# Kernel tuning notes

Hardware: AMD Instinct MI355X
Metric: run time of the kernel (lower is better)

Reference implementation:

```python
import jax, jax.numpy as jnp
import numpy as np

N, E = 50000, 800000
IN_DIM, HID, ZDIM = 256, 128, 64
LN_EPS = 1e-5


def _layernorm(x, gamma, beta):
    mu = jnp.mean(x, axis=-1, keepdims=True)
    var = jnp.mean(jnp.square(x - mu), axis=-1, keepdims=True)
    return (x - mu) * jax.lax.rsqrt(var + LN_EPS) * gamma + beta


def _gcn_conv(h, src, dst, dinv, W, b):
    # h: (N, d_in) -> (N, d_out). GCNConv: X W, then sym-normalized
    # aggregation over edges with self-loops, then bias.
    h = h @ W                                   # (N, d_out)
    coef = dinv[src] * dinv[dst]                # (E,)
    agg = jax.ops.segment_sum(h[src] * coef[:, None], dst,
                              num_segments=h.shape[0])
    agg = agg + h * jnp.square(dinv)[:, None]   # self-loop term
    return agg + b


def setup_inputs() -> dict:
    key = jax.random.key(0)
    ks = jax.random.split(key, 5)
    x = jax.random.normal(ks[0], (N, IN_DIM), dtype=jnp.float32)
    edge_index = jax.random.randint(ks[1], (2, E), 0, N, dtype=jnp.int64)
    s1 = 1.0 / np.sqrt(IN_DIM)
    s2 = 1.0 / np.sqrt(HID)
    return {
        "x": x,
        "edge_index": edge_index,
        "ln_gamma": jnp.ones((IN_DIM,), jnp.float32),
        "ln_beta": jnp.zeros((IN_DIM,), jnp.float32),
        "W1": jax.random.normal(ks[2], (IN_DIM, HID), jnp.float32) * s1,
        "b1": jnp.zeros((HID,), jnp.float32),
        "W2": jax.random.normal(ks[3], (HID, HID), jnp.float32) * s2,
        "b2": jnp.zeros((HID,), jnp.float32),
        "W3": jax.random.normal(ks[4], (HID, ZDIM), jnp.float32) * s2,
        "b3": jnp.zeros((ZDIM,), jnp.float32),
    }


def reference(x, edge_index, ln_gamma, ln_beta, W1, b1, W2, b2, W3, b3):
    src, dst = edge_index[0], edge_index[1]
    n = x.shape[0]
    # degree with self-loops (dropout is inference no-op, training=False)
    deg = jnp.ones((n,), x.dtype).at[dst].add(1.0)
    dinv = jax.lax.rsqrt(deg)
    h = _layernorm(x, ln_gamma, ln_beta)
    h = jax.nn.relu(_gcn_conv(h, src, dst, dinv, W1, b1))
    h = jax.nn.relu(_gcn_conv(h, src, dst, dinv, W2, b2))
    z = _gcn_conv(h, src, dst, dinv, W3, b3)
    return z
```

## Files before the change

kernel.cpp:

```cpp
#include <hip/hip_runtime.h>
#include <cstdint>
#include <cstddef>


typedef __attribute__((ext_vector_type(8))) __bf16 bf16x8;
typedef __attribute__((ext_vector_type(4))) float f32x4;
typedef _Float16 half_t;
typedef __attribute__((ext_vector_type(8))) _Float16 half8_t;

__global__ void zero_ctl(int* __restrict__ p, int n) {
  int i = blockIdx.x * 256 + threadIdx.x;
  if (i < n) p[i] = 0;
}

__global__ __launch_bounds__(256) void hist_bucket(const int* __restrict__ dst,
                                                   int* __restrict__ bcnt, int E, int NB) {
  __shared__ int h[256];
  int t = threadIdx.x;
  h[t] = 0;
  __syncthreads();
  for (int e = blockIdx.x * 256 + t; e < E; e += gridDim.x * 256)
    atomicAdd(&h[dst[e] >> 8], 1);
  __syncthreads();
  if (t < NB && h[t]) atomicAdd(&bcnt[t], h[t]);
}

__global__ __launch_bounds__(256) void scan_buckets(const int* __restrict__ bcnt,
                                                    int* __restrict__ bbase,
                                                    int* __restrict__ bcur, int NB, int E) {
  __shared__ int tmp[256];
  int t = threadIdx.x;
  int v = (t < NB) ? bcnt[t] : 0;
  tmp[t] = v;
  __syncthreads();
  for (int off = 1; off < 256; off <<= 1) {
    int x = (t >= off) ? tmp[t - off] : 0;
    __syncthreads();
    tmp[t] += x;
    __syncthreads();
  }
  int excl = tmp[t] - v;
  if (t < NB) { bbase[t] = excl; bcur[t] = excl; }
  if (t == 0) bbase[NB] = E;
}

#define CHUNK 4096
__global__ __launch_bounds__(256) void scatter_bins(const int* __restrict__ src,
                                                    const int* __restrict__ dst,
                                                    int* __restrict__ bcur,
                                                    int2* __restrict__ binned, int E) {
  __shared__ int2 recs[CHUNK];
  __shared__ int hist[256], lbase[256], resv[256], cur[256];
  int t = threadIdx.x;
  int e0 = blockIdx.x * CHUNK;
  if (e0 >= E) return;
  int len = min(CHUNK, E - e0);
  hist[t] = 0;
  cur[t] = 0;
  __syncthreads();
  for (int i = t; i < len; i += 256) atomicAdd(&hist[dst[e0 + i] >> 8], 1);
  __syncthreads();
  int v = hist[t];
  lbase[t] = v;
  __syncthreads();
  for (int off = 1; off < 256; off <<= 1) {
    int x = (t >= off) ? lbase[t - off] : 0;
    __syncthreads();
    lbase[t] += x;
    __syncthreads();
  }
  int myexcl = lbase[t] - v;
  if (v) resv[t] = atomicAdd(&bcur[t], v);
  __syncthreads();
  lbase[t] = myexcl;
  __syncthreads();
  for (int i = t; i < len; i += 256) {
    int d = dst[e0 + i], s = src[e0 + i];
    int b = d >> 8;
    int r = atomicAdd(&cur[b], 1);
    recs[lbase[b] + r] = make_int2(s, d);
  }
  __syncthreads();
  for (int i = t; i < len; i += 256) {
    int2 rc = recs[i];
    int b = rc.y >> 8;
    binned[resv[b] + (i - lbase[b])] = rc;
  }
}

#define MAXB 8192
__global__ __launch_bounds__(256) void sort_bucket(const int2* __restrict__ binned,
                                                   const int* __restrict__ bbase,
                                                   int* __restrict__ srcs,
                                                   int* __restrict__ offs,
                                                   float* __restrict__ dinv,
                                                   int N, int NB, int E) {
  __shared__ int2 recs[MAXB];
  __shared__ unsigned short rnk[MAXB];
  __shared__ int sstage[MAXB];
  __shared__ int hist[256], nbase[256];
  int b = blockIdx.x, t = threadIdx.x;
  int base = bbase[b], end = bbase[b + 1];
  int L = end - base;
  if (L > MAXB) L = MAXB;
  hist[t] = 0;
  __syncthreads();
  for (int i = t; i < L; i += 256) {
    int2 rc = binned[base + i];
    recs[i] = rc;
    int r = atomicAdd(&hist[rc.y & 255], 1);
    rnk[i] = (unsigned short)r;
  }
  __syncthreads();
  int v = hist[t];
  nbase[t] = v;
  __syncthreads();
  for (int off = 1; off < 256; off <<= 1) {
    int x = (t >= off) ? nbase[t - off] : 0;
    __syncthreads();
    nbase[t] += x;
    __syncthreads();
  }
  int excl = nbase[t] - v;
  __syncthreads();
  nbase[t] = excl;
  int node = (b << 8) + t;
  if (node < N) {
    offs[node] = base + excl;
    dinv[node] = rsqrtf(1.0f + (float)v);
  }
  if (b == NB - 1 && t == 0) offs[N] = E;
  __syncthreads();
  for (int i = t; i < L; i += 256) {
    int2 rc = recs[i];
    sstage[nbase[rc.y & 255] + rnk[i]] = rc.x;
  }
  __syncthreads();
  for (int i = t; i < L; i += 256) srcs[base + i] = sstage[i];
}

__global__ void fill_w(const int* __restrict__ srcs, const float* __restrict__ dinv,
                       int2* __restrict__ edges, int E) {
  int e = blockIdx.x * 256 + threadIdx.x;
  if (e < E) {
    int s = srcs[e];
    edges[e] = make_int2(s, __float_as_int(dinv[s]));
  }
}

__global__ void ln_stats(const float* __restrict__ x, float* __restrict__ mu,
                         float* __restrict__ rs, int n) {
  int gid = blockIdx.x * blockDim.x + threadIdx.x;
  int wv = gid >> 6, lane = gid & 63;
  if (wv >= n) return;
  const float4* row = (const float4*)(x + (size_t)wv * 256);
  float4 v = row[lane];
  float s = v.x + v.y + v.z + v.w;
  float s2 = v.x * v.x + v.y * v.y + v.z * v.z + v.w * v.w;
  for (int off = 32; off > 0; off >>= 1) {
    s += __shfl_down(s, off);
    s2 += __shfl_down(s2, off);
  }
  if (lane == 0) {
    float m = s * (1.0f / 256.0f);
    float var = s2 * (1.0f / 256.0f) - m * m;
    mu[wv] = m;
    rs[wv] = rsqrtf(var + 1e-5f);
  }
}

__global__ void wsplit(const float* __restrict__ W, unsigned short* __restrict__ Wt_hi,
                       unsigned short* __restrict__ Wt_lo, int K, int NOUT) {
  int idx = blockIdx.x * 256 + threadIdx.x;
  if (idx >= K * NOUT) return;
  int k = idx / NOUT, n = idx % NOUT;
  float v = W[idx];
  __bf16 h = (__bf16)v;
  __bf16 l = (__bf16)(v - (float)h);
  Wt_hi[(size_t)n * K + k] = __builtin_bit_cast(unsigned short, h);
  Wt_lo[(size_t)n * K + k] = __builtin_bit_cast(unsigned short, l);
}

template <int K, int NOUT, bool LN, bool A_FP16>
__launch_bounds__(256)
__global__ void gemm_mfma(const void* __restrict__ Avoid,
                          const unsigned short* __restrict__ Wt_hi,
                          const unsigned short* __restrict__ Wt_lo,
                          const float* __restrict__ mu, const float* __restrict__ rs,
                          const float* __restrict__ gamma, const float* __restrict__ beta,
                          half_t* __restrict__ out, int nrows) {
  constexpr int BM = 64, BK = 32;
  constexpr int NT = NOUT / 16;
  __shared__ unsigned short As_hi[BM][BK];
  __shared__ unsigned short As_lo[BM][BK];
  __shared__ unsigned short Bs_hi[NOUT][BK];
  __shared__ unsigned short Bs_lo[NOUT][BK];

  const int tid = threadIdx.x;
  const int lane = tid & 63;
  const int w = tid >> 6;
  const int quad = lane >> 4;
  const int l16 = lane & 15;
  const int row0 = blockIdx.x * BM;

  f32x4 acc[NT];
#pragma unroll
  for (int t = 0; t < NT; ++t) acc[t] = (f32x4){0.f, 0.f, 0.f, 0.f};

  for (int k0 = 0; k0 < K; k0 += BK) {
    if (!A_FP16) {
      const float* A = (const float*)Avoid;
#pragma unroll
      for (int i = 0; i < 2; ++i) {
        int r = i * 32 + (tid >> 3);
        int c4 = (tid & 7) * 4;
        int grow = row0 + r;
        if (grow > nrows - 1) grow = nrows - 1;
        float4 v = *(const float4*)&A[(size_t)grow * K + k0 + c4];
        if (LN) {
          float m = mu[grow], s = rs[grow];
          float4 g = *(const float4*)&gamma[k0 + c4];
          float4 b = *(const float4*)&beta[k0 + c4];
          v.x = (v.x - m) * s * g.x + b.x;
          v.y = (v.y - m) * s * g.y + b.y;
          v.z = (v.z - m) * s * g.z + b.z;
          v.w = (v.w - m) * s * g.w + b.w;
        }
        float vv[4] = {v.x, v.y, v.z, v.w};
#pragma unroll
        for (int j = 0; j < 4; ++j) {
          __bf16 h = (__bf16)vv[j];
          __bf16 l = (__bf16)(vv[j] - (float)h);
          As_hi[r][c4 + j] = __builtin_bit_cast(unsigned short, h);
          As_lo[r][c4 + j] = __builtin_bit_cast(unsigned short, l);
        }
      }
    } else {
      const half_t* A = (const half_t*)Avoid;
      int r = tid >> 2;
      int c8 = (tid & 3) * 8;
      int grow = row0 + r;
      if (grow > nrows - 1) grow = nrows - 1;
      half8_t v = *(const half8_t*)&A[(size_t)grow * K + k0 + c8];
#pragma unroll
      for (int j = 0; j < 8; ++j) {
        float f = (float)v[j];
        __bf16 h = (__bf16)f;
        __bf16 l = (__bf16)(f - (float)h);
        As_hi[r][c8 + j] = __builtin_bit_cast(unsigned short, h);
        As_lo[r][c8 + j] = __builtin_bit_cast(unsigned short, l);
      }
    }
#pragma unroll
    for (int i = 0; i < NOUT / 64; ++i) {
      int n = i * 64 + (tid >> 2);
      int c8 = (tid & 3) * 8;
      *(uint4*)&Bs_hi[n][c8] = *(const uint4*)&Wt_hi[(size_t)n * K + k0 + c8];
      *(uint4*)&Bs_lo[n][c8] = *(const uint4*)&Wt_lo[(size_t)n * K + k0 + c8];
    }
    __syncthreads();

    bf16x8 ah = *(const bf16x8*)&As_hi[w * 16 + l16][quad * 8];
    bf16x8 al = *(const bf16x8*)&As_lo[w * 16 + l16][quad * 8];
#pragma unroll
    for (int t = 0; t < NT; ++t) {
      bf16x8 bh = *(const bf16x8*)&Bs_hi[t * 16 + l16][quad * 8];
      bf16x8 bl = *(const bf16x8*)&Bs_lo[t * 16 + l16][quad * 8];
      acc[t] = __builtin_amdgcn_mfma_f32_16x16x32_bf16(ah, bh, acc[t], 0, 0, 0);
      acc[t] = __builtin_amdgcn_mfma_f32_16x16x32_bf16(al, bh, acc[t], 0, 0, 0);
      acc[t] = __builtin_amdgcn_mfma_f32_16x16x32_bf16(ah, bl, acc[t], 0, 0, 0);
    }
    __syncthreads();
  }

#pragma unroll
  for (int t = 0; t < NT; ++t) {
#pragma unroll
    for (int r = 0; r < 4; ++r) {
      int grow = row0 + w * 16 + quad * 4 + r;
      if (grow < nrows) out[(size_t)grow * NOUT + t * 16 + l16] = (half_t)acc[t][r];
    }
  }
}

__global__ __launch_bounds__(256) void agg128_h(const half_t* __restrict__ t,
                                                const int* __restrict__ offs,
                                                const int2* __restrict__ edges,
                                                const float* __restrict__ dinv,
                                                const float* __restrict__ bias,
                                                half_t* __restrict__ out, int n) {
  int gid = blockIdx.x * blockDim.x + threadIdx.x;
  int node = gid >> 6, lane = gid & 63;
  if (node >= n) return;
  int qw = lane >> 4;
  int fl = lane & 15;
  int e0 = offs[node], e1 = offs[node + 1];
  float acc[8] = {0.f, 0.f, 0.f, 0.f, 0.f, 0.f, 0.f, 0.f};
  int e = e0 + qw;
  for (; e + 12 < e1; e += 16) {
    int2 da = edges[e], db = edges[e + 4], dc = edges[e + 8], dd = edges[e + 12];
    half8_t va = *(const half8_t*)(t + ((size_t)da.x << 7) + fl * 8);
    half8_t vb = *(const half8_t*)(t + ((size_t)db.x << 7) + fl * 8);
    half8_t vc = *(const half8_t*)(t + ((size_t)dc.x << 7) + fl * 8);
    half8_t vd = *(const half8_t*)(t + ((size_t)dd.x << 7) + fl * 8);
    float wa = __int_as_float(da.y), wb = __int_as_float(db.y);
    float wc = __int_as_float(dc.y), wd = __int_as_float(dd.y);
#pragma unroll
    for (int j = 0; j < 8; ++j) {
      acc[j] = fmaf(wa, (float)va[j], acc[j]);
      acc[j] = fmaf(wb, (float)vb[j], acc[j]);
      acc[j] = fmaf(wc, (float)vc[j], acc[j]);
      acc[j] = fmaf(wd, (float)vd[j], acc[j]);
    }
  }
  for (; e < e1; e += 4) {
    int2 d = edges[e];
    half8_t v = *(const half8_t*)(t + ((size_t)d.x << 7) + fl * 8);
    float w = __int_as_float(d.y);
#pragma unroll
    for (int j = 0; j < 8; ++j) acc[j] = fmaf(w, (float)v[j], acc[j]);
  }
#pragma unroll
  for (int j = 0; j < 8; ++j) {
    acc[j] += __shfl_xor(acc[j], 16);
    acc[j] += __shfl_xor(acc[j], 32);
  }
  if (qw == 0) {
    float di = dinv[node];
    float dii = di * di;
    half8_t sv = *(const half8_t*)(t + ((size_t)node << 7) + fl * 8);
    float4 b0 = *(const float4*)(bias + fl * 8);
    float4 b1 = *(const float4*)(bias + fl * 8 + 4);
    float bb[8] = {b0.x, b0.y, b0.z, b0.w, b1.x, b1.y, b1.z, b1.w};
    half8_t o;
#pragma unroll
    for (int j = 0; j < 8; ++j) {
      float v = di * acc[j] + dii * (float)sv[j] + bb[j];
      o[j] = (half_t)fmaxf(v, 0.f);
    }
    *(half8_t*)(out + ((size_t)node << 7) + fl * 8) = o;
  }
}

__global__ __launch_bounds__(256) void agg64_h(const half_t* __restrict__ t,
                                               const int* __restrict__ offs,
                                               const int2* __restrict__ edges,
                                               const float* __restrict__ dinv,
                                               const float* __restrict__ bias,
                                               float* __restrict__ out, int n) {
  int gid = blockIdx.x * blockDim.x + threadIdx.x;
  int node = gid >> 6, lane = gid & 63;
  if (node >= n) return;
  int og = lane >> 3;
  int fl = lane & 7;
  int e0 = offs[node], e1 = offs[node + 1];
  float acc[8] = {0.f, 0.f, 0.f, 0.f, 0.f, 0.f, 0.f, 0.f};
  int e = e0 + og;
  for (; e + 8 < e1; e += 16) {
    int2 da = edges[e], db = edges[e + 8];
    half8_t va = *(const half8_t*)(t + ((size_t)da.x << 6) + fl * 8);
    half8_t vb = *(const half8_t*)(t + ((size_t)db.x << 6) + fl * 8);
    float wa = __int_as_float(da.y), wb = __int_as_float(db.y);
#pragma unroll
    for (int j = 0; j < 8; ++j) {
      acc[j] = fmaf(wa, (float)va[j], acc[j]);
      acc[j] = fmaf(wb, (float)vb[j], acc[j]);
    }
  }
  for (; e < e1; e += 8) {
    int2 d = edges[e];
    half8_t v = *(const half8_t*)(t + ((size_t)d.x << 6) + fl * 8);
    float w = __int_as_float(d.y);
#pragma unroll
    for (int j = 0; j < 8; ++j) acc[j] = fmaf(w, (float)v[j], acc[j]);
  }
#pragma unroll
  for (int j = 0; j < 8; ++j) {
    acc[j] += __shfl_xor(acc[j], 8);
    acc[j] += __shfl_xor(acc[j], 16);
    acc[j] += __shfl_xor(acc[j], 32);
  }
  if (og == 0) {
    float di = dinv[node];
    float dii = di * di;
    half8_t sv = *(const half8_t*)(t + ((size_t)node << 6) + fl * 8);
    float4 b0 = *(const float4*)(bias + fl * 8);
    float4 b1 = *(const float4*)(bias + fl * 8 + 4);
    float bb[8] = {b0.x, b0.y, b0.z, b0.w, b1.x, b1.y, b1.z, b1.w};
    float4 o0, o1;
    float ov[8];
#pragma unroll
    for (int j = 0; j < 8; ++j) ov[j] = di * acc[j] + dii * (float)sv[j] + bb[j];
    o0 = make_float4(ov[0], ov[1], ov[2], ov[3]);
    o1 = make_float4(ov[4], ov[5], ov[6], ov[7]);
    *(float4*)(out + ((size_t)node << 6) + fl * 8) = o0;
    *(float4*)(out + ((size_t)node << 6) + fl * 8 + 4) = o1;
  }
}

extern "C" void kernel_launch(void* const* d_in, const int* in_sizes, int n_in,
                              void* d_out, int out_size, void* d_ws, size_t ws_size,
                              hipStream_t stream) {
  const float* x = (const float*)d_in[0];
  const int* ei = (const int*)d_in[1];
  const float* gamma = (const float*)d_in[2];
  const float* beta = (const float*)d_in[3];
  const float* W1 = (const float*)d_in[4];
  const float* b1 = (const float*)d_in[5];
  const float* W2 = (const float*)d_in[6];
  const float* b2 = (const float*)d_in[7];
  const float* W3 = (const float*)d_in[8];
  const float* b3 = (const float*)d_in[9];
  float* out = (float*)d_out;

  const int N = in_sizes[0] / 256;
  const int E = in_sizes[1] / 2;
  const int* src = ei;
  const int* dst = ei + E;
  const int NB = (N + 255) >> 8;

  char* ws = (char*)d_ws;
  auto alloc = [&](size_t bytes) -> char* {
    char* p = ws;
    ws += (bytes + 255) & ~(size_t)255;
    return p;
  };
  int* bcnt = (int*)alloc(256 * 4);
  int* bbase = (int*)alloc(257 * 4);
  int* bcur = (int*)alloc(256 * 4);
  int2* binned = (int2*)alloc((size_t)E * 8);
  int* srcs = (int*)alloc((size_t)E * 4);
  int* offs = (int*)alloc((size_t)(N + 1) * 4);
  float* dinv = (float*)alloc((size_t)N * 4);
  int2* edges = (int2*)alloc((size_t)E * 8);
  float* mu = (float*)alloc((size_t)N * 4);
  float* rs = (float*)alloc((size_t)N * 4);
  half_t* t = (half_t*)alloc((size_t)N * 128 * 2);
  half_t* h = (half_t*)alloc((size_t)N * 128 * 2);
  unsigned short* W1t_hi = (unsigned short*)alloc(256 * 128 * 2);
  unsigned short* W1t_lo = (unsigned short*)alloc(256 * 128 * 2);
  unsigned short* W2t_hi = (unsigned short*)alloc(128 * 128 * 2);
  unsigned short* W2t_lo = (unsigned short*)alloc(128 * 128 * 2);
  unsigned short* W3t_hi = (unsigned short*)alloc(128 * 64 * 2);
  unsigned short* W3t_lo = (unsigned short*)alloc(128 * 64 * 2);

  zero_ctl<<<1, 256, 0, stream>>>(bcnt, 256);
  hist_bucket<<<256, 256, 0, stream>>>(dst, bcnt, E, NB);
  scan_buckets<<<1, 256, 0, stream>>>(bcnt, bbase, bcur, NB, E);
  scatter_bins<<<(E + CHUNK - 1) / CHUNK, 256, 0, stream>>>(src, dst, bcur, binned, E);
  sort_bucket<<<NB, 256, 0, stream>>>(binned, bbase, srcs, offs, dinv, N, NB, E);
  fill_w<<<(E + 255) / 256, 256, 0, stream>>>(srcs, dinv, edges, E);

  wsplit<<<(256 * 128 + 255) / 256, 256, 0, stream>>>(W1, W1t_hi, W1t_lo, 256, 128);
  wsplit<<<(128 * 128 + 255) / 256, 256, 0, stream>>>(W2, W2t_hi, W2t_lo, 128, 128);
  wsplit<<<(128 * 64 + 255) / 256, 256, 0, stream>>>(W3, W3t_hi, W3t_lo, 128, 64);

  ln_stats<<<(N + 3) / 4, 256, 0, stream>>>(x, mu, rs, N);

  const int gemm_blocks = (N + 63) / 64;
  const int agg_blocks = (N + 3) / 4;

  gemm_mfma<256, 128, true, false><<<gemm_blocks, 256, 0, stream>>>(
      x, W1t_hi, W1t_lo, mu, rs, gamma, beta, t, N);
  agg128_h<<<agg_blocks, 256, 0, stream>>>(t, offs, edges, dinv, b1, h, N);

  gemm_mfma<128, 128, false, true><<<gemm_blocks, 256, 0, stream>>>(
      h, W2t_hi, W2t_lo, nullptr, nullptr, nullptr, nullptr, t, N);
  agg128_h<<<agg_blocks, 256, 0, stream>>>(t, offs, edges, dinv, b2, h, N);

  gemm_mfma<128, 64, false, true><<<gemm_blocks, 256, 0, stream>>>(
      h, W3t_hi, W3t_lo, nullptr, nullptr, nullptr, nullptr, t, N);
  agg64_h<<<agg_blocks, 256, 0, stream>>>(t, offs, edges, dinv, b3, out, N);
}
```

Before: 301.8 us.

## Fuse LN stats into GEMM, fold edge weights into sort, merge weight splits

Layer-norm row statistics are now computed inside the first GEMM block from the tile's own rows, which removes the separate ln_stats pass and the mu/rs arrays. Degrees are counted with global atomics during the histogram pass so dinv is ready before sorting. That lets sort_bucket write (src, dinv[src]) edge records directly and drops the fill_w kernel and the srcs buffer. The three weight-split launches are merged into one. In exchange, the GEMM re-reads each row of x once more per block and the histogram pass gains per-node global atomics.

```diff
diff --git a/kernel.cpp b/kernel.cpp
--- a/kernel.cpp
+++ b/kernel.cpp
@@ -13,14 +13,18 @@
   if (i < n) p[i] = 0;
 }
 
-__global__ __launch_bounds__(256) void hist_bucket(const int* __restrict__ dst,
-                                                   int* __restrict__ bcnt, int E, int NB) {
+__global__ __launch_bounds__(256) void histdeg(const int* __restrict__ dst,
+                                               int* __restrict__ bcnt,
+                                               int* __restrict__ cnt, int E, int NB) {
   __shared__ int h[256];
   int t = threadIdx.x;
   h[t] = 0;
   __syncthreads();
-  for (int e = blockIdx.x * 256 + t; e < E; e += gridDim.x * 256)
-    atomicAdd(&h[dst[e] >> 8], 1);
+  for (int e = blockIdx.x * 256 + t; e < E; e += gridDim.x * 256) {
+    int d = dst[e];
+    atomicAdd(&h[d >> 8], 1);
+    atomicAdd(&cnt[d], 1);
+  }
   __syncthreads();
   if (t < NB && h[t]) atomicAdd(&bcnt[t], h[t]);
 }
@@ -42,6 +46,11 @@
   int excl = tmp[t] - v;
   if (t < NB) { bbase[t] = excl; bcur[t] = excl; }
   if (t == 0) bbase[NB] = E;
+}
+
+__global__ void dinv_fin(const int* __restrict__ cnt, float* __restrict__ dinv, int n) {
+  int i = blockIdx.x * 256 + threadIdx.x;
+  if (i < n) dinv[i] = rsqrtf(1.0f + (float)cnt[i]);
 }
 
 #define CHUNK 4096
@@ -91,9 +100,9 @@
 #define MAXB 8192
 __global__ __launch_bounds__(256) void sort_bucket(const int2* __restrict__ binned,
                                                    const int* __restrict__ bbase,
-                                                   int* __restrict__ srcs,
+                                                   const float* __restrict__ dinv,
+                                                   int2* __restrict__ edges,
                                                    int* __restrict__ offs,
-                                                   float* __restrict__ dinv,
                                                    int N, int NB, int E) {
   __shared__ int2 recs[MAXB];
   __shared__ unsigned short rnk[MAXB];
@@ -125,10 +134,7 @@
   __syncthreads();
   nbase[t] = excl;
   int node = (b << 8) + t;
-  if (node < N) {
-    offs[node] = base + excl;
-    dinv[node] = rsqrtf(1.0f + (float)v);
-  }
+  if (node < N) offs[node] = base + excl;
   if (b == NB - 1 && t == 0) offs[N] = E;
   __syncthreads();
   for (int i = t; i < L; i += 256) {
@@ -136,49 +142,38 @@
     sstage[nbase[rc.y & 255] + rnk[i]] = rc.x;
   }
   __syncthreads();
-  for (int i = t; i < L; i += 256) srcs[base + i] = sstage[i];
-}
-
-__global__ void fill_w(const int* __restrict__ srcs, const float* __restrict__ dinv,
-                       int2* __restrict__ edges, int E) {
-  int e = blockIdx.x * 256 + threadIdx.x;
-  if (e < E) {
-    int s = srcs[e];
-    edges[e] = make_int2(s, __float_as_int(dinv[s]));
-  }
-}
-
-__global__ void ln_stats(const float* __restrict__ x, float* __restrict__ mu,
-                         float* __restrict__ rs, int n) {
-  int gid = blockIdx.x * blockDim.x + threadIdx.x;
-  int wv = gid >> 6, lane = gid & 63;
-  if (wv >= n) return;
-  const float4* row = (const float4*)(x + (size_t)wv * 256);
-  float4 v = row[lane];
-  float s = v.x + v.y + v.z + v.w;
-  float s2 = v.x * v.x + v.y * v.y + v.z * v.z + v.w * v.w;
-  for (int off = 32; off > 0; off >>= 1) {
-    s += __shfl_down(s, off);
-    s2 += __shfl_down(s2, off);
-  }
-  if (lane == 0) {
-    float m = s * (1.0f / 256.0f);
-    float var = s2 * (1.0f / 256.0f) - m * m;
-    mu[wv] = m;
-    rs[wv] = rsqrtf(var + 1e-5f);
-  }
-}
-
-__global__ void wsplit(const float* __restrict__ W, unsigned short* __restrict__ Wt_hi,
-                       unsigned short* __restrict__ Wt_lo, int K, int NOUT) {
+  for (int i = t; i < L; i += 256) {
+    int s = sstage[i];
+    edges[base + i] = make_int2(s, __float_as_int(dinv[s]));
+  }
+}
+
+__global__ void wsplit_all(const float* __restrict__ W1, const float* __restrict__ W2,
+                           const float* __restrict__ W3,
+                           unsigned short* __restrict__ W1t_hi, unsigned short* __restrict__ W1t_lo,
+                           unsigned short* __restrict__ W2t_hi, unsigned short* __restrict__ W2t_lo,
+                           unsigned short* __restrict__ W3t_hi, unsigned short* __restrict__ W3t_lo) {
   int idx = blockIdx.x * 256 + threadIdx.x;
-  if (idx >= K * NOUT) return;
+  const float* W;
+  unsigned short *Th, *Tl;
+  int K, NOUT;
+  if (idx < 32768) {
+    W = W1; Th = W1t_hi; Tl = W1t_lo; K = 256; NOUT = 128;
+  } else if (idx < 49152) {
+    idx -= 32768;
+    W = W2; Th = W2t_hi; Tl = W2t_lo; K = 128; NOUT = 128;
+  } else if (idx < 57344) {
+    idx -= 49152;
+    W = W3; Th = W3t_hi; Tl = W3t_lo; K = 128; NOUT = 64;
+  } else {
+    return;
+  }
   int k = idx / NOUT, n = idx % NOUT;
   float v = W[idx];
   __bf16 h = (__bf16)v;
   __bf16 l = (__bf16)(v - (float)h);
-  Wt_hi[(size_t)n * K + k] = __builtin_bit_cast(unsigned short, h);
-  Wt_lo[(size_t)n * K + k] = __builtin_bit_cast(unsigned short, l);
+  Th[(size_t)n * K + k] = __builtin_bit_cast(unsigned short, h);
+  Tl[(size_t)n * K + k] = __builtin_bit_cast(unsigned short, l);
 }
 
 template <int K, int NOUT, bool LN, bool A_FP16>
@@ -186,7 +181,6 @@
 __global__ void gemm_mfma(const void* __restrict__ Avoid,
                           const unsigned short* __restrict__ Wt_hi,
                           const unsigned short* __restrict__ Wt_lo,
-                          const float* __restrict__ mu, const float* __restrict__ rs,
                           const float* __restrict__ gamma, const float* __restrict__ beta,
                           half_t* __restrict__ out, int nrows) {
   constexpr int BM = 64, BK = 32;
@@ -195,6 +189,7 @@
   __shared__ unsigned short As_lo[BM][BK];
   __shared__ unsigned short Bs_hi[NOUT][BK];
   __shared__ unsigned short Bs_lo[NOUT][BK];
+  __shared__ float smu[BM], srs[BM];
 
   const int tid = threadIdx.x;
   const int lane = tid & 63;
@@ -202,6 +197,35 @@
   const int quad = lane >> 4;
   const int l16 = lane & 15;
   const int row0 = blockIdx.x * BM;
+
+  if (LN && !A_FP16) {
+    __shared__ float sred[4][BM];
+    __shared__ float sred2[4][BM];
+    const float* A = (const float*)Avoid;
+    int r = tid & 63, seg = tid >> 6;
+    int grow = row0 + r;
+    if (grow > nrows - 1) grow = nrows - 1;
+    const float* Arow = A + (size_t)grow * K + seg * 64;
+    float s = 0.f, s2 = 0.f;
+#pragma unroll
+    for (int c = 0; c < 64; c += 4) {
+      float4 v = *(const float4*)&Arow[c];
+      s += v.x + v.y + v.z + v.w;
+      s2 += v.x * v.x + v.y * v.y + v.z * v.z + v.w * v.w;
+    }
+    sred[seg][r] = s;
+    sred2[seg][r] = s2;
+    __syncthreads();
+    if (tid < BM) {
+      float ss = sred[0][tid] + sred[1][tid] + sred[2][tid] + sred[3][tid];
+      float ss2 = sred2[0][tid] + sred2[1][tid] + sred2[2][tid] + sred2[3][tid];
+      float m = ss * (1.0f / 256.0f);
+      float var = ss2 * (1.0f / 256.0f) - m * m;
+      smu[tid] = m;
+      srs[tid] = rsqrtf(var + 1e-5f);
+    }
+    __syncthreads();
+  }
 
   f32x4 acc[NT];
 #pragma unroll
@@ -218,7 +242,7 @@
         if (grow > nrows - 1) grow = nrows - 1;
         float4 v = *(const float4*)&A[(size_t)grow * K + k0 + c4];
         if (LN) {
-          float m = mu[grow], s = rs[grow];
+          float m = smu[r], s = srs[r];
           float4 g = *(const float4*)&gamma[k0 + c4];
           float4 b = *(const float4*)&beta[k0 + c4];
           v.x = (v.x - m) * s * g.x + b.x;
@@ -387,14 +411,11 @@
     float4 b0 = *(const float4*)(bias + fl * 8);
     float4 b1 = *(const float4*)(bias + fl * 8 + 4);
     float bb[8] = {b0.x, b0.y, b0.z, b0.w, b1.x, b1.y, b1.z, b1.w};
-    float4 o0, o1;
     float ov[8];
 #pragma unroll
     for (int j = 0; j < 8; ++j) ov[j] = di * acc[j] + dii * (float)sv[j] + bb[j];
-    o0 = make_float4(ov[0], ov[1], ov[2], ov[3]);
-    o1 = make_float4(ov[4], ov[5], ov[6], ov[7]);
-    *(float4*)(out + ((size_t)node << 6) + fl * 8) = o0;
-    *(float4*)(out + ((size_t)node << 6) + fl * 8 + 4) = o1;
+    *(float4*)(out + ((size_t)node << 6) + fl * 8) = make_float4(ov[0], ov[1], ov[2], ov[3]);
+    *(float4*)(out + ((size_t)node << 6) + fl * 8 + 4) = make_float4(ov[4], ov[5], ov[6], ov[7]);
   }
 }
 
@@ -425,16 +446,14 @@
     ws += (bytes + 255) & ~(size_t)255;
     return p;
   };
-  int* bcnt = (int*)alloc(256 * 4);
+  int* cnt = (int*)alloc((size_t)(N + 256) * 4);
+  int* bcnt = cnt + N;
   int* bbase = (int*)alloc(257 * 4);
   int* bcur = (int*)alloc(256 * 4);
   int2* binned = (int2*)alloc((size_t)E * 8);
-  int* srcs = (int*)alloc((size_t)E * 4);
   int* offs = (int*)alloc((size_t)(N + 1) * 4);
   float* dinv = (float*)alloc((size_t)N * 4);
   int2* edges = (int2*)alloc((size_t)E * 8);
-  float* mu = (float*)alloc((size_t)N * 4);
-  float* rs = (float*)alloc((size_t)N * 4);
   half_t* t = (half_t*)alloc((size_t)N * 128 * 2);
   half_t* h = (half_t*)alloc((size_t)N * 128 * 2);
   unsigned short* W1t_hi = (unsigned short*)alloc(256 * 128 * 2);
@@ -444,31 +463,28 @@
   unsigned short* W3t_hi = (unsigned short*)alloc(128 * 64 * 2);
   unsigned short* W3t_lo = (unsigned short*)alloc(128 * 64 * 2);
 
-  zero_ctl<<<1, 256, 0, stream>>>(bcnt, 256);
-  hist_bucket<<<256, 256, 0, stream>>>(dst, bcnt, E, NB);
+  zero_ctl<<<(N + 256 + 255) / 256, 256, 0, stream>>>(cnt, N + 256);
+  histdeg<<<256, 256, 0, stream>>>(dst, bcnt, cnt, E, NB);
   scan_buckets<<<1, 256, 0, stream>>>(bcnt, bbase, bcur, NB, E);
+  dinv_fin<<<(N + 255) / 256, 256, 0, stream>>>(cnt, dinv, N);
   scatter_bins<<<(E + CHUNK - 1) / CHUNK, 256, 0, stream>>>(src, dst, bcur, binned, E);
-  sort_bucket<<<NB, 256, 0, stream>>>(binned, bbase, srcs, offs, dinv, N, NB, E);
-  fill_w<<<(E + 255) / 256, 256, 0, stream>>>(srcs, dinv, edges, E);
-
-  wsplit<<<(256 * 128 + 255) / 256, 256, 0, stream>>>(W1, W1t_hi, W1t_lo, 256, 128);
-  wsplit<<<(128 * 128 + 255) / 256, 256, 0, stream>>>(W2, W2t_hi, W2t_lo, 128, 128);
-  wsplit<<<(128 * 64 + 255) / 256, 256, 0, stream>>>(W3, W3t_hi, W3t_lo, 128, 64);
-
-  ln_stats<<<(N + 3) / 4, 256, 0, stream>>>(x, mu, rs, N);
+  sort_bucket<<<NB, 256, 0, stream>>>(binned, bbase, dinv, edges, offs, N, NB, E);
+
+  wsplit_all<<<(57344 + 255) / 256, 256, 0, stream>>>(W1, W2, W3, W1t_hi, W1t_lo,
+                                                      W2t_hi, W2t_lo, W3t_hi, W3t_lo);
 
   const int gemm_blocks = (N + 63) / 64;
   const int agg_blocks = (N + 3) / 4;
 
   gemm_mfma<256, 128, true, false><<<gemm_blocks, 256, 0, stream>>>(
-      x, W1t_hi, W1t_lo, mu, rs, gamma, beta, t, N);
+      x, W1t_hi, W1t_lo, gamma, beta, t, N);
   agg128_h<<<agg_blocks, 256, 0, stream>>>(t, offs, edges, dinv, b1, h, N);
 
   gemm_mfma<128, 128, false, true><<<gemm_blocks, 256, 0, stream>>>(
-      h, W2t_hi, W2t_lo, nullptr, nullptr, nullptr, nullptr, t, N);
+      h, W2t_hi, W2t_lo, nullptr, nullptr, t, N);
   agg128_h<<<agg_blocks, 256, 0, stream>>>(t, offs, edges, dinv, b2, h, N);
 
   gemm_mfma<128, 64, false, true><<<gemm_blocks, 256, 0, stream>>>(
-      h, W3t_hi, W3t_lo, nullptr, nullptr, nullptr, nullptr, t, N);
+      h, W3t_hi, W3t_lo, nullptr, nullptr, t, N);
   agg64_h<<<agg_blocks, 256, 0, stream>>>(t, offs, edges, dinv, b3, out, N);
 }
```

Result: slower. 322.5 us (+6.9%).
